# Kernel optimization log

Measured on AMD Instinct MI355X. Metric: run time of the kernel, lower is better.

## Reference

```python
import jax, jax.numpy as jnp
import numpy as np

B, S, D = 2, 2048, 1024
H = 16
HD = D // H  # 64

def setup_inputs() -> dict:
    key = jax.random.key(0)
    ks = jax.random.split(key, 5)
    scale = 0.02
    x = jax.random.normal(ks[0], (B, S, D), dtype=jnp.float32)
    w_attn = jax.random.normal(ks[1], (D, 3 * D), dtype=jnp.float32) * scale
    b_attn = jnp.zeros((3 * D,), dtype=jnp.float32)
    w_proj = jax.random.normal(ks[2], (D, D), dtype=jnp.float32) * scale
    b_proj = jnp.zeros((D,), dtype=jnp.float32)
    return {"x": x, "w_attn": w_attn, "b_attn": b_attn, "w_proj": w_proj, "b_proj": b_proj}

def reference(x, w_attn, b_attn, w_proj, b_proj):
    b, s, d = x.shape
    qkv = x @ w_attn + b_attn                      # [B,S,3D]
    q, k, v = jnp.split(qkv, 3, axis=-1)
    # [B,H,S,HD]
    q = q.reshape(b, s, H, HD).transpose(0, 2, 1, 3)
    k = k.reshape(b, s, H, HD).transpose(0, 2, 1, 3)
    v = v.reshape(b, s, H, HD).transpose(0, 2, 1, 3)
    scores = jnp.einsum('bhqd,bhkd->bhqk', q, k) * (1.0 / np.sqrt(HD))
    causal = jnp.tril(jnp.ones((s, s), dtype=bool))
    scores = jnp.where(causal[None, None], scores, -jnp.inf)
    attn = jax.nn.softmax(scores, axis=-1)
    out = jnp.einsum('bhqk,bhkd->bhqd', attn, v)   # [B,H,S,HD]
    out = out.transpose(0, 2, 1, 3).reshape(b, s, d)
    return out @ w_proj + b_proj
```

## Files before the change

kernel.cpp:

```cpp
#include <hip/hip_runtime.h>

#define B_  2
#define S_  2048
#define D_  1024
#define H_  16
#define HD_ 64
#define TD_ 3072
#define M_  (B_*S_)
#define NWORK_ 24

using bf16x8 = __attribute__((ext_vector_type(8))) short;
using bf16x4 = __attribute__((ext_vector_type(4))) short;
using f32x4  = __attribute__((ext_vector_type(4))) float;

typedef __attribute__((address_space(1))) unsigned int uint_g;
typedef __attribute__((address_space(3))) unsigned int uint_l;

#define MFMA32 __builtin_amdgcn_mfma_f32_16x16x32_bf16

#if defined(__has_builtin)
#if __has_builtin(__builtin_amdgcn_mfma_f32_16x16x16_bf16_1k)
#define MFMA16(a,b,c) __builtin_amdgcn_mfma_f32_16x16x16_bf16_1k(a,b,c,0,0,0)
#define HAVE_MFMA16 1
#elif __has_builtin(__builtin_amdgcn_mfma_f32_16x16x16bf16_1k)
#define MFMA16(a,b,c) __builtin_amdgcn_mfma_f32_16x16x16bf16_1k(a,b,c,0,0,0)
#define HAVE_MFMA16 1
#endif
#endif
#ifndef HAVE_MFMA16
static __device__ __forceinline__ f32x4 MFMA16_stub(bf16x4 a, bf16x4 b, f32x4 c) { return c; }
#define MFMA16(a,b,c) MFMA16_stub(a,b,c)
#endif

static __device__ __forceinline__ short f2bf(float f) {
    unsigned u = __float_as_uint(f);
    u += 0x7FFFu + ((u >> 16) & 1u);
    return (short)(u >> 16);
}
static __device__ __forceinline__ unsigned pack2bf(float a, float b) {
    return (unsigned)(unsigned short)f2bf(a) | ((unsigned)(unsigned short)f2bf(b) << 16);
}
static __device__ __forceinline__ void gload_lds16(const short* g, short* l) {
    __builtin_amdgcn_global_load_lds((const uint_g*)g, (uint_l*)l, 16, 0, 0);
}
static __device__ __forceinline__ void unpack8(uint4 u, float* f) {
    unsigned a0 = u.x, a1 = u.y, a2 = u.z, a3 = u.w;
    f[0] = __uint_as_float(a0 << 16); f[1] = __uint_as_float(a0 & 0xFFFF0000u);
    f[2] = __uint_as_float(a1 << 16); f[3] = __uint_as_float(a1 & 0xFFFF0000u);
    f[4] = __uint_as_float(a2 << 16); f[5] = __uint_as_float(a2 & 0xFFFF0000u);
    f[6] = __uint_as_float(a3 << 16); f[7] = __uint_as_float(a3 & 0xFFFF0000u);
}

__global__ void cast_x_kernel(const float* __restrict__ x, short* __restrict__ xb, int n4) {
    int i = blockIdx.x * blockDim.x + threadIdx.x;
    if (i >= n4) return;
    float4 v = *((const float4*)x + i);
    short4 o;
    o.x = f2bf(v.x); o.y = f2bf(v.y); o.z = f2bf(v.z); o.w = f2bf(v.w);
    *((short4*)xb + i) = o;
}

__global__ __launch_bounds__(256)
void wtrans_kernel(const float* __restrict__ W, short* __restrict__ Wt, int K, int N) {
    __shared__ float T[32][33];
    int n0 = blockIdx.x * 32, k0 = blockIdx.y * 32;
    int tx = threadIdx.x & 31, ty = threadIdx.x >> 5;
    #pragma unroll
    for (int i = 0; i < 4; ++i)
        T[ty + i * 8][tx] = W[(size_t)(k0 + ty + i * 8) * N + n0 + tx];
    __syncthreads();
    #pragma unroll
    for (int i = 0; i < 4; ++i)
        Wt[(size_t)(n0 + ty + i * 8) * K + k0 + tx] = f2bf(T[tx][ty + i * 8]);
}

__global__ __launch_bounds__(256)
void vtrans_kernel(const short* __restrict__ V, short* __restrict__ Vt) {
    __shared__ short T[32][33];
    int p  = blockIdx.z;
    int s0 = blockIdx.x * 32;
    int d0 = blockIdx.y * 32;
    int tx = threadIdx.x & 31, ty = threadIdx.x >> 5;
    const short* Vp  = V  + (size_t)p * S_ * HD_;
    short*       Vtp = Vt + (size_t)p * HD_ * S_;
    #pragma unroll
    for (int i = 0; i < 4; ++i)
        T[ty + i * 8][tx] = Vp[(s0 + ty + i * 8) * HD_ + d0 + tx];
    __syncthreads();
    #pragma unroll
    for (int i = 0; i < 4; ++i)
        Vtp[(size_t)(d0 + ty + i * 8) * S_ + s0 + tx] = T[tx][ty + i * 8];
}

__global__ __launch_bounds__(512, 2)
void gemm256_qkv_kernel(const short* __restrict__ A, const short* __restrict__ Bt,
                        const float* __restrict__ bias,
                        short* __restrict__ Qo, short* __restrict__ Ko, short* __restrict__ Vo,
                        int M, int N, int K) {
    __shared__ __align__(16) char lds[131072];

    const int tid  = threadIdx.x;
    const int w    = tid >> 6, lane = tid & 63;
    const int quad = lane >> 4, l16 = lane & 15;
    const int wm   = w >> 2,  wn  = w & 3;

    const int gx  = gridDim.x;
    const int nwg = gx * gridDim.y;
    const int bid = blockIdx.y * gx + blockIdx.x;
    const int sbid = (bid & 7) * (nwg >> 3) + (bid >> 3);
    const int rowBase = (sbid / gx) * 256;
    const int colBase = (sbid % gx) * 256;

    const int scol = ((lane & 3) * 8) ^ ((lane & 32) >> 1);
    const int sr0  = (w * 2) * 16 + (lane >> 2);
    const short* Asrc0 = A  + (size_t)(rowBase + sr0)      * K + scol;
    const short* Asrc1 = A  + (size_t)(rowBase + sr0 + 16) * K + scol;
    const short* Bsrc0 = Bt + (size_t)(colBase + sr0)      * K + scol;
    const short* Bsrc1 = Bt + (size_t)(colBase + sr0 + 16) * K + scol;

    const int rterm = (l16 * 64 + quad * 16) ^ ((l16 & 8) << 2);
    const char* ArdBase = lds + wm * 8192 + rterm;
    const char* BrdBase = lds + 65536 + wn * 4096 + rterm;

#define STAGE_A(t) { int sl_ = ((t) & 3) * 16384; \
    gload_lds16(Asrc0 + (size_t)(t) * 32, (short*)(lds + sl_) + (w * 2)     * 512); \
    gload_lds16(Asrc1 + (size_t)(t) * 32, (short*)(lds + sl_) + (w * 2 + 1) * 512); }
#define STAGE_B(t) { int sl_ = 65536 + ((t) & 3) * 16384; \
    gload_lds16(Bsrc0 + (size_t)(t) * 32, (short*)(lds + sl_) + (w * 2)     * 512); \
    gload_lds16(Bsrc1 + (size_t)(t) * 32, (short*)(lds + sl_) + (w * 2 + 1) * 512); }

    f32x4 acc[8][4];
    const f32x4 zero = {0.f, 0.f, 0.f, 0.f};
    #pragma unroll
    for (int i = 0; i < 8; ++i)
        #pragma unroll
        for (int j = 0; j < 4; ++j) acc[i][j] = zero;

    const int nk = K >> 5;
    STAGE_A(0); STAGE_B(0);
    STAGE_A(1); STAGE_B(1);

    for (int t = 0; t < nk; ++t) {
        if (t + 1 < nk) { asm volatile("s_waitcnt vmcnt(4)" ::: "memory"); }
        else            { asm volatile("s_waitcnt vmcnt(0)" ::: "memory"); }
        __builtin_amdgcn_s_barrier();
        __builtin_amdgcn_sched_barrier(0);

        const char* Ab = ArdBase + (t & 3) * 16384;
        const char* Bb = BrdBase + (t & 3) * 16384;
        bf16x8 bfr[4], afr[4];
        #pragma unroll
        for (int ni = 0; ni < 4; ++ni) bfr[ni] = *(const bf16x8*)(Bb + ni * 1024);
        #pragma unroll
        for (int mi = 0; mi < 4; ++mi) afr[mi] = *(const bf16x8*)(Ab + mi * 1024);
        if (t + 2 < nk) STAGE_A(t + 2);

        __builtin_amdgcn_s_setprio(1);
        #pragma unroll
        for (int mi = 0; mi < 4; ++mi)
            #pragma unroll
            for (int ni = 0; ni < 4; ++ni)
                acc[mi][ni] = MFMA32(afr[mi], bfr[ni], acc[mi][ni], 0, 0, 0);
        __builtin_amdgcn_s_setprio(0);

        #pragma unroll
        for (int mi = 0; mi < 4; ++mi) afr[mi] = *(const bf16x8*)(Ab + (4 + mi) * 1024);
        if (t + 2 < nk) STAGE_B(t + 2);

        __builtin_amdgcn_s_setprio(1);
        #pragma unroll
        for (int mi = 0; mi < 4; ++mi)
            #pragma unroll
            for (int ni = 0; ni < 4; ++ni)
                acc[4 + mi][ni] = MFMA32(afr[mi], bfr[ni], acc[4 + mi][ni], 0, 0, 0);
        __builtin_amdgcn_s_setprio(0);
    }
#undef STAGE_A
#undef STAGE_B

    #pragma unroll
    for (int ni = 0; ni < 4; ++ni) {
        int col = colBase + wn * 64 + ni * 16 + l16;
        int sel = col >> 10, cr = col & 1023;
        int h = cr >> 6, d = cr & 63;
        float bv  = bias[col];
        short* dst = (sel == 0) ? Qo : (sel == 1) ? Ko : Vo;
        float  scl = (sel == 0) ? 0.125f * 1.44269504f : 1.0f;
        #pragma unroll
        for (int mi = 0; mi < 8; ++mi) {
            int row = rowBase + wm * 128 + mi * 16 + quad * 4;
            #pragma unroll
            for (int r = 0; r < 4; ++r) {
                int rw = row + r;
                int bb = rw >> 11, s = rw & 2047;
                dst[((size_t)(bb * H_ + h) * S_ + s) * HD_ + d] =
                    f2bf((acc[mi][ni][r] + bv) * scl);
            }
        }
    }
}

template<int MODE>
__global__ __launch_bounds__(256)
void gemm_mfma_kernel(const short* __restrict__ A, const short* __restrict__ Bt,
                      const float* __restrict__ bias, float* __restrict__ Cf,
                      short* __restrict__ Qo, short* __restrict__ Ko, short* __restrict__ Vo,
                      int M, int N, int K) {
    __shared__ __align__(16) short As[128 * 32];
    __shared__ __align__(16) short Bs[128 * 32];

    const int tid  = threadIdx.x;
    const int w    = tid >> 6, lane = tid & 63;
    const int quad = lane >> 4, l16 = lane & 15;
    const int wr = (w >> 1) * 64, wc = (w & 1) * 64;
    const int rowBase = blockIdx.y * 128, colBase = blockIdx.x * 128;

    f32x4 acc[4][4];
    const f32x4 zero = {0.f, 0.f, 0.f, 0.f};
    #pragma unroll
    for (int i = 0; i < 4; ++i)
        #pragma unroll
        for (int j = 0; j < 4; ++j) acc[i][j] = zero;

    const int srow = lane >> 2;
    const int scol = (lane & 3) * 8;

    for (int k0 = 0; k0 < K; k0 += 32) {
        __syncthreads();
        gload_lds16(A  + (size_t)(rowBase + w * 16 + srow)      * K + k0 + scol, &As[(w * 16) * 32]);
        gload_lds16(A  + (size_t)(rowBase + 64 + w * 16 + srow) * K + k0 + scol, &As[(64 + w * 16) * 32]);
        gload_lds16(Bt + (size_t)(colBase + w * 16 + srow)      * K + k0 + scol, &Bs[(w * 16) * 32]);
        gload_lds16(Bt + (size_t)(colBase + 64 + w * 16 + srow) * K + k0 + scol, &Bs[(64 + w * 16) * 32]);
        __syncthreads();

        bf16x8 af[4], bf[4];
        #pragma unroll
        for (int t = 0; t < 4; ++t) {
            af[t] = *(const bf16x8*)&As[(wr + t * 16 + l16) * 32 + quad * 8];
            bf[t] = *(const bf16x8*)&Bs[(wc + t * 16 + l16) * 32 + quad * 8];
        }
        #pragma unroll
        for (int i = 0; i < 4; ++i)
            #pragma unroll
            for (int j = 0; j < 4; ++j)
                acc[i][j] = MFMA32(af[i], bf[j], acc[i][j], 0, 0, 0);
    }

    if (MODE == 0) {
        #pragma unroll
        for (int i = 0; i < 4; ++i) {
            int row = rowBase + wr + i * 16 + quad * 4;
            #pragma unroll
            for (int j = 0; j < 4; ++j) {
                int col = colBase + wc + j * 16 + l16;
                float bv = bias[col];
                #pragma unroll
                for (int r = 0; r < 4; ++r)
                    Cf[(size_t)(row + r) * N + col] = acc[i][j][r] + bv;
            }
        }
    } else {
        #pragma unroll
        for (int j = 0; j < 4; ++j) {
            int col = colBase + wc + j * 16 + l16;
            int sel = col >> 10, cr = col & 1023;
            int h = cr >> 6, d = cr & 63;
            float bv  = bias[col];
            short* dst = (sel == 0) ? Qo : (sel == 1) ? Ko : Vo;
            float  scl = (sel == 0) ? 0.125f * 1.44269504f : 1.0f;
            #pragma unroll
            for (int i = 0; i < 4; ++i) {
                int row = rowBase + wr + i * 16 + quad * 4;
                #pragma unroll
                for (int r = 0; r < 4; ++r) {
                    int rw = row + r;
                    int bb = rw >> 11, s = rw & 2047;
                    dst[((size_t)(bb * H_ + h) * S_ + s) * HD_ + d] =
                        f2bf((acc[i][j][r] + bv) * scl);
                }
            }
        }
    }
}

__global__ __launch_bounds__(256, 3)
void flash_mfma_kernel(const short* __restrict__ Qg, const short* __restrict__ Kg,
                       const short* __restrict__ Vtg,
                       short* __restrict__ pO, float* __restrict__ pl) {
    __shared__ __align__(16) short Ks[64][72];
    __shared__ __align__(16) short Vs[64][72];

    const int plane_id = blockIdx.x;
    const int y = blockIdx.y;
    int qi, kc;
    if (y < 8) { qi = y; kc = 0; }
    else       { qi = 8 + ((y - 8) >> 1); kc = (y - 8) & 1; }
    int nkt = 2 * qi + 2 - kc * 16;
    if (nkt > 16) nkt = 16;
    const int kvOrigin = kc * 1024;

    const int tid  = threadIdx.x;
    const int w    = tid >> 6, lane = tid & 63;
    const int quad = lane >> 4, l16 = lane & 15;
    const int qBase = qi * 128;
    const size_t plane = (size_t)plane_id * S_ * HD_;

    const int sr0 = tid >> 3;
    const int sc0 = (tid & 7) * 8;

    const int qsubA = qBase + w * 32;
    const short* QrowA = Qg + plane + (size_t)(qsubA + l16) * HD_ + quad * 8;
    const bf16x8 qa0 = *(const bf16x8*)(QrowA);
    const bf16x8 qa1 = *(const bf16x8*)(QrowA + 32);
    const short* QrowB = QrowA + 16 * HD_;
    const bf16x8 qb0 = *(const bf16x8*)(QrowB);
    const bf16x8 qb1 = *(const bf16x8*)(QrowB + 32);

    f32x4 oA[4], oB[4];
    const f32x4 zero = {0.f, 0.f, 0.f, 0.f};
    #pragma unroll
    for (int i = 0; i < 4; ++i) { oA[i] = zero; oB[i] = zero; }
    float lA = 0.f, lB = 0.f;
    const int q_globA = qsubA + l16;
    const int q_globB = qsubA + 16 + l16;
    const int q_wave_max = qsubA + 31;

    uint4 ka0, ka1, va0, va1;
    ka0 = *(const uint4*)(Kg  + plane + (size_t)(kvOrigin + sr0)      * HD_ + sc0);
    ka1 = *(const uint4*)(Kg  + plane + (size_t)(kvOrigin + sr0 + 32) * HD_ + sc0);
    va0 = *(const uint4*)(Vtg + plane + (size_t)sr0        * S_ + kvOrigin + sc0);
    va1 = *(const uint4*)(Vtg + plane + (size_t)(sr0 + 32) * S_ + kvOrigin + sc0);

    for (int j = 0; j < nkt; ++j) {
        __syncthreads();
        *(uint4*)&Ks[sr0][sc0]      = ka0;
        *(uint4*)&Ks[sr0 + 32][sc0] = ka1;
        *(uint4*)&Vs[sr0][sc0]      = va0;
        *(uint4*)&Vs[sr0 + 32][sc0] = va1;
        __syncthreads();

        if (j + 1 < nkt) {
            const int kvB = kvOrigin + (j + 1) * 64;
            ka0 = *(const uint4*)(Kg  + plane + (size_t)(kvB + sr0)      * HD_ + sc0);
            ka1 = *(const uint4*)(Kg  + plane + (size_t)(kvB + sr0 + 32) * HD_ + sc0);
            va0 = *(const uint4*)(Vtg + plane + (size_t)sr0        * S_ + kvB + sc0);
            va1 = *(const uint4*)(Vtg + plane + (size_t)(sr0 + 32) * S_ + kvB + sc0);
        }

        const int kvBase = kvOrigin + j * 64;
        if (kvBase > q_wave_max) continue;

        f32x4 sA[4], sB[4];
        __builtin_amdgcn_s_setprio(1);
        #pragma unroll
        for (int ct = 0; ct < 4; ++ct) {
            bf16x8 kf0 = *(const bf16x8*)&Ks[ct * 16 + l16][quad * 8];
            bf16x8 kf1 = *(const bf16x8*)&Ks[ct * 16 + l16][32 + quad * 8];
            f32x4 a = zero, b = zero;
            a = MFMA32(kf0, qa0, a, 0, 0, 0);
            a = MFMA32(kf1, qa1, a, 0, 0, 0);
            b = MFMA32(kf0, qb0, b, 0, 0, 0);
            b = MFMA32(kf1, qb1, b, 0, 0, 0);
            sA[ct] = a; sB[ct] = b;
        }
        __builtin_amdgcn_s_setprio(0);

        if (kvBase + 63 > qsubA) {
            #pragma unroll
            for (int ct = 0; ct < 4; ++ct) {
                int kv = kvBase + ct * 16 + quad * 4;
                #pragma unroll
                for (int r = 0; r < 4; ++r)
                    if (kv + r > q_globA) sA[ct][r] = -3.0e38f;
            }
        }
        if (kvBase + 63 > qsubA + 16) {
            #pragma unroll
            for (int ct = 0; ct < 4; ++ct) {
                int kv = kvBase + ct * 16 + quad * 4;
                #pragma unroll
                for (int r = 0; r < 4; ++r)
                    if (kv + r > q_globB) sB[ct][r] = -3.0e38f;
            }
        }

        #pragma unroll
        for (int ct = 0; ct < 4; ++ct) {
            float pa0 = __builtin_amdgcn_exp2f(sA[ct][0]), pa1 = __builtin_amdgcn_exp2f(sA[ct][1]);
            float pa2 = __builtin_amdgcn_exp2f(sA[ct][2]), pa3 = __builtin_amdgcn_exp2f(sA[ct][3]);
            float pb0 = __builtin_amdgcn_exp2f(sB[ct][0]), pb1 = __builtin_amdgcn_exp2f(sB[ct][1]);
            float pb2 = __builtin_amdgcn_exp2f(sB[ct][2]), pb3 = __builtin_amdgcn_exp2f(sB[ct][3]);
            lA += (pa0 + pa1) + (pa2 + pa3);
            lB += (pb0 + pb1) + (pb2 + pb3);
            bf16x4 pA, pB;
            *(unsigned*)&pA       = pack2bf(pa0, pa1);
            *((unsigned*)&pA + 1) = pack2bf(pa2, pa3);
            *(unsigned*)&pB       = pack2bf(pb0, pb1);
            *((unsigned*)&pB + 1) = pack2bf(pb2, pb3);
            __builtin_amdgcn_s_setprio(1);
            #pragma unroll
            for (int dt = 0; dt < 4; ++dt) {
                bf16x4 vfr = *(const bf16x4*)&Vs[dt * 16 + l16][ct * 16 + quad * 4];
                oA[dt] = MFMA16(vfr, pA, oA[dt]);
                oB[dt] = MFMA16(vfr, pB, oB[dt]);
            }
            __builtin_amdgcn_s_setprio(0);
        }
    }

    lA += __shfl_xor(lA, 16); lA += __shfl_xor(lA, 32);
    lB += __shfl_xor(lB, 16); lB += __shfl_xor(lB, 32);
    const size_t lbase = ((size_t)plane_id * NWORK_ + y) * 128 + w * 32;
    if (quad == 0) {
        pl[lbase + l16]      = lA;
        pl[lbase + 16 + l16] = lB;
    }

    __syncthreads();
    short* Pw = (w < 2) ? &Ks[w * 32][0] : &Vs[(w - 2) * 32][0];
    #pragma unroll
    for (int dt = 0; dt < 4; ++dt) {
        uint2 ua, ub;
        ua.x = pack2bf(oA[dt][0], oA[dt][1]);
        ua.y = pack2bf(oA[dt][2], oA[dt][3]);
        ub.x = pack2bf(oB[dt][0], oB[dt][1]);
        ub.y = pack2bf(oB[dt][2], oB[dt][3]);
        *(uint2*)&Pw[l16 * 72 + dt * 16 + quad * 4]        = ua;
        *(uint2*)&Pw[(16 + l16) * 72 + dt * 16 + quad * 4] = ub;
    }
    __builtin_amdgcn_s_waitcnt(0xC07F);
    short* outBase = pO + (((size_t)plane_id * NWORK_ + y) * 128 + w * 32) * 64;
    #pragma unroll
    for (int pass = 0; pass < 4; ++pass) {
        int r  = pass * 8 + (lane >> 3);
        int cs = (lane & 7) * 8;
        uint4 vv = *(const uint4*)&Pw[r * 72 + cs];
        *(uint4*)(outBase + r * 64 + cs) = vv;
    }
}

__global__ __launch_bounds__(256)
void reduce_kernel(const short* __restrict__ pO, const float* __restrict__ pl,
                   short* __restrict__ atb) {
    const int plane_id = blockIdx.x, qi = blockIdx.y;
    const int h = plane_id & (H_ - 1), b = plane_id >> 4;
    const int tid = threadIdx.x;
    const int row = tid >> 1;
    const int cb  = (tid & 1) * 32;

    int t0, nch;
    if (qi < 8) { t0 = qi; nch = 1; }
    else        { t0 = 8 + 2 * (qi - 8); nch = 2; }

    const size_t pbase = (((size_t)plane_id * NWORK_ + t0) * 128 + row) * 64 + cb;
    float f[32], g[8];
    unpack8(*(const uint4*)(pO + pbase),      f);
    unpack8(*(const uint4*)(pO + pbase + 8),  f + 8);
    unpack8(*(const uint4*)(pO + pbase + 16), f + 16);
    unpack8(*(const uint4*)(pO + pbase + 24), f + 24);
    float l = pl[((size_t)plane_id * NWORK_ + t0) * 128 + row];
    if (nch == 2) {
        #pragma unroll
        for (int c = 0; c < 4; ++c) {
            unpack8(*(const uint4*)(pO + pbase + 8192 + c * 8), g);
            #pragma unroll
            for (int i = 0; i < 8; ++i) f[c * 8 + i] += g[i];
        }
        l += pl[((size_t)plane_id * NWORK_ + t0 + 1) * 128 + row];
    }
    const float inv = 1.0f / l;
    short* dst = atb + (size_t)(b * S_ + qi * 128 + row) * D_ + h * HD_ + cb;
    #pragma unroll
    for (int c = 0; c < 4; ++c) {
        uint2 o2;
        o2.x = pack2bf(f[c * 8 + 0] * inv, f[c * 8 + 1] * inv);
        o2.y = pack2bf(f[c * 8 + 2] * inv, f[c * 8 + 3] * inv);
        uint2 o3;
        o3.x = pack2bf(f[c * 8 + 4] * inv, f[c * 8 + 5] * inv);
        o3.y = pack2bf(f[c * 8 + 6] * inv, f[c * 8 + 7] * inv);
        uint4 ov; ov.x = o2.x; ov.y = o2.y; ov.z = o3.x; ov.w = o3.y;
        *(uint4*)(dst + c * 8) = ov;
    }
}

extern "C" void kernel_launch(void* const* d_in, const int* in_sizes, int n_in,
                              void* d_out, int out_size, void* d_ws, size_t ws_size,
                              hipStream_t stream) {
    const float* x      = (const float*)d_in[0];
    const float* w_attn = (const float*)d_in[1];
    const float* b_attn = (const float*)d_in[2];
    const float* w_proj = (const float*)d_in[3];
    const float* b_proj = (const float*)d_in[4];
    float* out = (float*)d_out;

    char* ws = (char*)d_ws;
    short* xb  = (short*)ws; ws += (size_t)M_ * D_ * 2;
    short* wat = (short*)ws; ws += (size_t)TD_ * D_ * 2;
    short* wpt = (short*)ws; ws += (size_t)D_ * D_ * 2;
    short* qg  = (short*)ws; ws += (size_t)M_ * D_ * 2;
    short* kg  = (short*)ws; ws += (size_t)M_ * D_ * 2;
    short* vg  = (short*)ws; ws += (size_t)M_ * D_ * 2;
    short* vtg = (short*)ws; ws += (size_t)M_ * D_ * 2;
    short* atb = (short*)ws; ws += (size_t)M_ * D_ * 2;

    short* pO = (short*)d_ws;
    float* pl = (float*)((char*)d_ws + (size_t)32 * NWORK_ * 128 * 64 * 2);

    cast_x_kernel<<<(M_ * D_ / 4 + 255) / 256, 256, 0, stream>>>(x, xb, M_ * D_ / 4);
    wtrans_kernel<<<dim3(TD_ / 32, D_ / 32), 256, 0, stream>>>(w_attn, wat, D_, TD_);
    wtrans_kernel<<<dim3(D_ / 32, D_ / 32), 256, 0, stream>>>(w_proj, wpt, D_, D_);

    gemm256_qkv_kernel<<<dim3(TD_ / 256, M_ / 256), 512, 0, stream>>>(
        xb, wat, b_attn, qg, kg, vg, M_, TD_, D_);

    vtrans_kernel<<<dim3(S_ / 32, HD_ / 32, B_ * H_), 256, 0, stream>>>(vg, vtg);

    flash_mfma_kernel<<<dim3(B_ * H_, NWORK_), 256, 0, stream>>>(qg, kg, vtg, pO, pl);

    reduce_kernel<<<dim3(B_ * H_, S_ / 128), 256, 0, stream>>>(pO, pl, atb);

    gemm_mfma_kernel<0><<<dim3(D_ / 128, M_ / 128), 256, 0, stream>>>(
        atb, wpt, b_proj, out, nullptr, nullptr, nullptr, M_, D_, D_);
}
```

Measured before the change: 193.2 us.

## Pipeline output projection GEMM with 4-slot LDS ring and swizzled layout

Replaces the simple two-barrier output projection GEMM with a kernel that prefetches two K-tiles ahead into a 4-slot LDS ring, waits with explicit vmcnt counters and a single barrier per step, and XOR-swizzles the LDS layout to avoid bank conflicts. It also remaps block IDs across 8 groups, likely to spread tiles over XCDs for cache locality, and raises MFMA priority. The aim is to hide global-load latency behind MFMA work in the final GEMM. The cost is 64KB of LDS per block, which limits occupancy to two blocks per CU. The unused MODE=1 QKV path is removed.

```diff
diff --git a/kernel.cpp b/kernel.cpp
--- a/kernel.cpp
+++ b/kernel.cpp
@@ -200,20 +200,41 @@
     }
 }
 
-template<int MODE>
-__global__ __launch_bounds__(256)
-void gemm_mfma_kernel(const short* __restrict__ A, const short* __restrict__ Bt,
-                      const float* __restrict__ bias, float* __restrict__ Cf,
-                      short* __restrict__ Qo, short* __restrict__ Ko, short* __restrict__ Vo,
-                      int M, int N, int K) {
-    __shared__ __align__(16) short As[128 * 32];
-    __shared__ __align__(16) short Bs[128 * 32];
+__global__ __launch_bounds__(256, 2)
+void gemm128_ring_kernel(const short* __restrict__ A, const short* __restrict__ Bt,
+                         const float* __restrict__ bias, float* __restrict__ Cf,
+                         int M, int N, int K) {
+    __shared__ __align__(16) char lds[65536];
 
     const int tid  = threadIdx.x;
     const int w    = tid >> 6, lane = tid & 63;
     const int quad = lane >> 4, l16 = lane & 15;
-    const int wr = (w >> 1) * 64, wc = (w & 1) * 64;
-    const int rowBase = blockIdx.y * 128, colBase = blockIdx.x * 128;
+    const int wm   = w >> 1,  wn  = w & 1;
+
+    const int gx  = gridDim.x;
+    const int nwg = gx * gridDim.y;
+    const int bid = blockIdx.y * gx + blockIdx.x;
+    const int sbid = (bid & 7) * (nwg >> 3) + (bid >> 3);
+    const int rowBase = (sbid / gx) * 128;
+    const int colBase = (sbid % gx) * 128;
+
+    const int scol = ((lane & 3) * 8) ^ ((lane & 32) >> 1);
+    const int sr0  = w * 32 + (lane >> 2);
+    const short* Asrc0 = A  + (size_t)(rowBase + sr0)      * K + scol;
+    const short* Asrc1 = A  + (size_t)(rowBase + sr0 + 16) * K + scol;
+    const short* Bsrc0 = Bt + (size_t)(colBase + sr0)      * K + scol;
+    const short* Bsrc1 = Bt + (size_t)(colBase + sr0 + 16) * K + scol;
+
+    const int rterm = (l16 * 64 + quad * 16) ^ ((l16 & 8) << 2);
+    const char* ArdBase = lds + wm * 4096 + rterm;
+    const char* BrdBase = lds + 32768 + wn * 4096 + rterm;
+
+#define STAGE_A(t) { int sl_ = ((t) & 3) * 8192; \
+    gload_lds16(Asrc0 + (size_t)(t) * 32, (short*)(lds + sl_) + (w * 2)     * 512); \
+    gload_lds16(Asrc1 + (size_t)(t) * 32, (short*)(lds + sl_) + (w * 2 + 1) * 512); }
+#define STAGE_B(t) { int sl_ = 32768 + ((t) & 3) * 8192; \
+    gload_lds16(Bsrc0 + (size_t)(t) * 32, (short*)(lds + sl_) + (w * 2)     * 512); \
+    gload_lds16(Bsrc1 + (size_t)(t) * 32, (short*)(lds + sl_) + (w * 2 + 1) * 512); }
 
     f32x4 acc[4][4];
     const f32x4 zero = {0.f, 0.f, 0.f, 0.f};
@@ -222,63 +243,46 @@
         #pragma unroll
         for (int j = 0; j < 4; ++j) acc[i][j] = zero;
 
-    const int srow = lane >> 2;
-    const int scol = (lane & 3) * 8;
-
-    for (int k0 = 0; k0 < K; k0 += 32) {
-        __syncthreads();
-        gload_lds16(A  + (size_t)(rowBase + w * 16 + srow)      * K + k0 + scol, &As[(w * 16) * 32]);
-        gload_lds16(A  + (size_t)(rowBase + 64 + w * 16 + srow) * K + k0 + scol, &As[(64 + w * 16) * 32]);
-        gload_lds16(Bt + (size_t)(colBase + w * 16 + srow)      * K + k0 + scol, &Bs[(w * 16) * 32]);
-        gload_lds16(Bt + (size_t)(colBase + 64 + w * 16 + srow) * K + k0 + scol, &Bs[(64 + w * 16) * 32]);
-        __syncthreads();
-
-        bf16x8 af[4], bf[4];
-        #pragma unroll
-        for (int t = 0; t < 4; ++t) {
-            af[t] = *(const bf16x8*)&As[(wr + t * 16 + l16) * 32 + quad * 8];
-            bf[t] = *(const bf16x8*)&Bs[(wc + t * 16 + l16) * 32 + quad * 8];
-        }
-        #pragma unroll
-        for (int i = 0; i < 4; ++i)
-            #pragma unroll
-            for (int j = 0; j < 4; ++j)
-                acc[i][j] = MFMA32(af[i], bf[j], acc[i][j], 0, 0, 0);
-    }
-
-    if (MODE == 0) {
-        #pragma unroll
-        for (int i = 0; i < 4; ++i) {
-            int row = rowBase + wr + i * 16 + quad * 4;
-            #pragma unroll
-            for (int j = 0; j < 4; ++j) {
-                int col = colBase + wc + j * 16 + l16;
-                float bv = bias[col];
-                #pragma unroll
-                for (int r = 0; r < 4; ++r)
-                    Cf[(size_t)(row + r) * N + col] = acc[i][j][r] + bv;
-            }
-        }
-    } else {
-        #pragma unroll
-        for (int j = 0; j < 4; ++j) {
-            int col = colBase + wc + j * 16 + l16;
-            int sel = col >> 10, cr = col & 1023;
-            int h = cr >> 6, d = cr & 63;
-            float bv  = bias[col];
-            short* dst = (sel == 0) ? Qo : (sel == 1) ? Ko : Vo;
-            float  scl = (sel == 0) ? 0.125f * 1.44269504f : 1.0f;
-            #pragma unroll
-            for (int i = 0; i < 4; ++i) {
-                int row = rowBase + wr + i * 16 + quad * 4;
-                #pragma unroll
-                for (int r = 0; r < 4; ++r) {
-                    int rw = row + r;
-                    int bb = rw >> 11, s = rw & 2047;
-                    dst[((size_t)(bb * H_ + h) * S_ + s) * HD_ + d] =
-                        f2bf((acc[i][j][r] + bv) * scl);
-                }
-            }
+    const int nk = K >> 5;
+    STAGE_A(0); STAGE_B(0);
+    STAGE_A(1); STAGE_B(1);
+
+    for (int t = 0; t < nk; ++t) {
+        if (t + 1 < nk) { asm volatile("s_waitcnt vmcnt(4)" ::: "memory"); }
+        else            { asm volatile("s_waitcnt vmcnt(0)" ::: "memory"); }
+        __builtin_amdgcn_s_barrier();
+        __builtin_amdgcn_sched_barrier(0);
+
+        const char* Ab = ArdBase + (t & 3) * 8192;
+        const char* Bb = BrdBase + (t & 3) * 8192;
+        bf16x8 bfr[4], afr[4];
+        #pragma unroll
+        for (int ni = 0; ni < 4; ++ni) bfr[ni] = *(const bf16x8*)(Bb + ni * 1024);
+        #pragma unroll
+        for (int mi = 0; mi < 4; ++mi) afr[mi] = *(const bf16x8*)(Ab + mi * 1024);
+        if (t + 2 < nk) { STAGE_A(t + 2); STAGE_B(t + 2); }
+
+        __builtin_amdgcn_s_setprio(1);
+        #pragma unroll
+        for (int mi = 0; mi < 4; ++mi)
+            #pragma unroll
+            for (int ni = 0; ni < 4; ++ni)
+                acc[mi][ni] = MFMA32(afr[mi], bfr[ni], acc[mi][ni], 0, 0, 0);
+        __builtin_amdgcn_s_setprio(0);
+    }
+#undef STAGE_A
+#undef STAGE_B
+
+    #pragma unroll
+    for (int mi = 0; mi < 4; ++mi) {
+        int row = rowBase + wm * 64 + mi * 16 + quad * 4;
+        #pragma unroll
+        for (int ni = 0; ni < 4; ++ni) {
+            int col = colBase + wn * 64 + ni * 16 + l16;
+            float bv = bias[col];
+            #pragma unroll
+            for (int r = 0; r < 4; ++r)
+                Cf[(size_t)(row + r) * N + col] = acc[mi][ni][r] + bv;
         }
     }
 }
@@ -519,6 +523,6 @@
 
     reduce_kernel<<<dim3(B_ * H_, S_ / 128), 256, 0, stream>>>(pO, pl, atb);
 
-    gemm_mfma_kernel<0><<<dim3(D_ / 128, M_ / 128), 256, 0, stream>>>(
-        atb, wpt, b_proj, out, nullptr, nullptr, nullptr, M_, D_, D_);
-}
+    gemm128_ring_kernel<<<dim3(D_ / 128, M_ / 128), 256, 0, stream>>>(
+        atb, wpt, b_proj, out, M_, D_, D_);
+}
```

New measurement: 179.4 us. 1.08x faster.
